# Optimization experiments

Measured on AMD Instinct MI355X. Metric: run time of the kernel, lower is better.

Reference implementation:

```python
import jax, jax.numpy as jnp
import numpy as np

GAMMA = 1.0

def setup_inputs() -> dict:
    key = jax.random.key(0)
    kq, kk, kv = jax.random.split(key, 3)
    B, N, M, D = 4, 2048, 2048, 128
    q = jax.random.normal(kq, (B, N, D), dtype=jnp.float32)
    k = jax.random.normal(kk, (B, M, D), dtype=jnp.float32)
    v = jax.random.normal(kv, (B, M, D), dtype=jnp.float32)
    return {"q": q, "k": k, "v": v}

def reference(q, k, v):
    # RBF attention: weights = softmax(-gamma * ||q_i - k_j||^2, axis=-1)
    # dist2 via expansion ||q||^2 + ||k||^2 - 2 q.k (same math as broadcast-subtract,
    # avoids materializing the [B,N,M,D] tensor the torch code builds).
    q2 = jnp.sum(q * q, axis=-1)                    # [B,N]
    k2 = jnp.sum(k * k, axis=-1)                    # [B,M]
    qk = jnp.einsum('bnd,bmd->bnm', q, k)           # [B,N,M]
    dist2 = q2[:, :, None] + k2[:, None, :] - 2.0 * qk
    weights = jax.nn.softmax(-GAMMA * dist2, axis=-1)  # [B,N,M]
    return jnp.einsum('bnm,bmd->bnd', weights, v)      # [B,N,D]
```

## Files before the change

### kernel.cpp

```cpp
#include <hip/hip_runtime.h>
#include <hip/hip_bf16.h>

#define B_ 4
#define N_ 2048
#define M_ 2048
#define D_ 128
#define QBLK 128
#define NTHREADS 256
#define KVBLK 64
#define NTILES 32
#define TILE_BYTES 16384
#define SPLIT_MAX 8
#define SCALE2LOG 2.885390081777927f
#define LOG2E 1.4426950408889634f
#define DEFER_THR 11.5424f

typedef __attribute__((ext_vector_type(8))) short short8;
typedef __attribute__((ext_vector_type(8))) _Float16 half8;
typedef __attribute__((ext_vector_type(16))) float floatx16;
typedef __attribute__((ext_vector_type(4))) unsigned int u32x4;
typedef unsigned short u16;
typedef unsigned int u32;

__device__ __forceinline__ u16 f2bf(float x) {
  u32 u = __builtin_bit_cast(u32, x);
  u32 r = (u + 0x7FFFu + ((u >> 16) & 1u)) >> 16;
  return (u16)r;
}
__device__ __forceinline__ float bf2f(u16 h) {
  u32 u = ((u32)h) << 16;
  return __builtin_bit_cast(float, u);
}
__device__ __forceinline__ u32 cvtpkh(float a, float b) {
  u32 r;
  asm("v_cvt_pkrtz_f16_f32 %0, %1, %2" : "=v"(r) : "v"(a), "v"(b));
  return r;
}

#define GLOAD16(src, dst)                                                     \
  __builtin_amdgcn_global_load_lds(                                           \
      (const __attribute__((address_space(1))) void*)(src),                   \
      (__attribute__((address_space(3))) void*)(dst), 16, 0, 0)

__global__ __launch_bounds__(256) void prep_kernel(
    const float* __restrict__ k, const float* __restrict__ v,
    u16* __restrict__ kf_g, u16* __restrict__ vt_g, float* __restrict__ k2_g)
{
  __shared__ u16 T[64][136];
  int tid = threadIdx.x;
  if (blockIdx.x < 512) {
    int gid = blockIdx.x * 256 + tid;
    int row_g = gid >> 4;
    int j = gid & 15;
    const float* kp = k + (size_t)row_g * D_ + j * 8;
    float4 a = *(const float4*)kp;
    float4 c = *(const float4*)(kp + 4);
    float xs[8] = {a.x, a.y, a.z, a.w, c.x, c.y, c.z, c.w};
    half8 kf;
    float ss = 0.f;
    #pragma unroll
    for (int e = 0; e < 8; ++e) {
      ss += xs[e] * xs[e];
      kf[e] = (_Float16)(SCALE2LOG * xs[e]);
    }
    ss += __shfl_xor(ss, 1);
    ss += __shfl_xor(ss, 2);
    ss += __shfl_xor(ss, 4);
    ss += __shfl_xor(ss, 8);
    if (j == 0) k2_g[row_g] = ss * LOG2E;
    int m = row_g & (M_ - 1);
    int b = row_g >> 11;
    int tile = m >> 6, r = m & 63;
    size_t base = ((size_t)b * NTILES + tile) * TILE_BYTES;
    u32 off = (u32)(r * 256 + j * 16) ^ ((u32)(r & 7) << 4);
    *(half8*)((char*)kf_g + base + off) = kf;
  } else {
    int blk = blockIdx.x - 512;
    int b = blk >> 5, tile = blk & 31;
    const float* vp = v + ((size_t)b * M_ + tile * 64) * D_;
    #pragma unroll
    for (int p = 0; p < 8; ++p) {
      int idx = p * 256 + tid;
      int r = idx >> 5, c4 = idx & 31;
      float4 vv = *(const float4*)(vp + (size_t)r * D_ + c4 * 4);
      T[r][c4 * 4 + 0] = __builtin_bit_cast(u16, (_Float16)vv.x);
      T[r][c4 * 4 + 1] = __builtin_bit_cast(u16, (_Float16)vv.y);
      T[r][c4 * 4 + 2] = __builtin_bit_cast(u16, (_Float16)vv.z);
      T[r][c4 * 4 + 3] = __builtin_bit_cast(u16, (_Float16)vv.w);
    }
    __syncthreads();
    size_t base = ((size_t)b * NTILES + tile) * TILE_BYTES;
    #pragma unroll
    for (int p = 0; p < 4; ++p) {
      int idx = p * 256 + tid;
      int d = idx >> 3, rb = idx & 7;
      short8 s;
      #pragma unroll
      for (int i = 0; i < 8; ++i) s[i] = (short)T[rb * 8 + i][d];
      u32 off = (u32)(d * 128 + rb * 16) ^ ((u32)(d & 7) << 4);
      *(short8*)((char*)vt_g + base + off) = s;
    }
  }
}

__global__ __launch_bounds__(NTHREADS, 2) void rbf_attn_kernel(
    const float* __restrict__ q, const u16* __restrict__ kf_g,
    const u16* __restrict__ vt_g, const float* __restrict__ k2_g,
    float* __restrict__ out, u16* __restrict__ Opart,
    float* __restrict__ mpart, float* __restrict__ lpart,
    int nsplit, int tiles_per_split)
{
  __shared__ __align__(16) u16 KfL[2][64 * 128];
  __shared__ __align__(16) u16 VtL[2][128 * 64];
  __shared__ __align__(16) float k2L[2][64];

  const int tid = threadIdx.x;
  const int w = tid >> 6;
  const int lane = tid & 63;
  const int qlc = lane & 31;
  const int h = lane >> 5;

  int b, qi, sp;
  {
    int gid = blockIdx.x;
    if (nsplit >= 2) {
      int xcd = gid & 7, slot = gid >> 3;
      int gpx = nsplit >> 1;
      int group = xcd * gpx + (slot >> 4);
      qi = slot & 15;
      b = group & 3;
      sp = group >> 2;
    } else {
      qi = gid & 15;
      b = gid >> 4;
      sp = 0;
    }
  }
  const int qt = qi;
  const int q0 = qt * QBLK;
  const int kt0 = sp * tiles_per_split, kt1 = kt0 + tiles_per_split;

  const char* kf_b = (const char*)kf_g + (size_t)b * NTILES * TILE_BYTES;
  const char* vt_b = (const char*)vt_g + (size_t)b * NTILES * TILE_BYTES;
  const float* k2_b = k2_g + (size_t)b * M_;
  const int so = tid * 16;

  #define STAGE(buf, kt)                                                      \
    do {                                                                      \
      const char* kh_ = kf_b + (size_t)(kt) * TILE_BYTES;                     \
      const char* vt_ = vt_b + (size_t)(kt) * TILE_BYTES;                     \
      char* dk = (char*)KfL[buf];                                             \
      char* dv = (char*)VtL[buf];                                             \
      _Pragma("unroll")                                                       \
      for (int c = 0; c < 4; ++c)                                             \
        GLOAD16(kh_ + c * 4096 + so, dk + c * 4096 + w * 1024);               \
      _Pragma("unroll")                                                       \
      for (int c = 0; c < 4; ++c)                                             \
        GLOAD16(vt_ + c * 4096 + so, dv + c * 4096 + w * 1024);               \
      if (tid < 16)                                                           \
        GLOAD16((const char*)(k2_b + (kt) * KVBLK) + tid * 16,                \
                (char*)k2L[buf]);                                             \
    } while (0)

  STAGE(0, kt0);

  half8 Qf[8];
  {
    const float* qp = q + ((size_t)b * N_ + q0 + w * 32 + qlc) * D_ + h * 8;
    #pragma unroll
    for (int s = 0; s < 8; ++s) {
      float4 a = *(const float4*)(qp + s * 16);
      float4 c = *(const float4*)(qp + s * 16 + 4);
      Qf[s][0] = (_Float16)a.x; Qf[s][1] = (_Float16)a.y;
      Qf[s][2] = (_Float16)a.z; Qf[s][3] = (_Float16)a.w;
      Qf[s][4] = (_Float16)c.x; Qf[s][5] = (_Float16)c.y;
      Qf[s][6] = (_Float16)c.z; Qf[s][7] = (_Float16)c.w;
    }
  }

  floatx16 o[4];
  #pragma unroll
  for (int dt = 0; dt < 4; ++dt) o[dt] = (floatx16)0.0f;
  float mrun = -1e30f, lrun = 0.f;

  asm volatile("s_waitcnt vmcnt(0)" ::: "memory");
  __syncthreads();

  int pb = 0;
  for (int kt = kt0; kt < kt1; ++kt) {
    if (kt + 1 < kt1) STAGE(pb ^ 1, kt + 1);

    const char* Kb = (const char*)KfL[pb];
    const char* Vb = (const char*)VtL[pb];
    const float* k2p = k2L[pb];

    floatx16 accS0 = (floatx16)0.0f, accS1 = (floatx16)0.0f;
    __builtin_amdgcn_s_setprio(1);
    #pragma unroll
    for (int s = 0; s < 8; ++s) {
      {
        int row = qlc;
        u32 off = ((u32)(row * 256 + s * 32 + h * 16)) ^ ((u32)(row & 7) << 4);
        half8 af = *(const half8*)(Kb + off);
        accS0 = __builtin_amdgcn_mfma_f32_32x32x16_f16(af, Qf[s], accS0, 0, 0, 0);
      }
      {
        int row = 32 + qlc;
        u32 off = ((u32)(row * 256 + s * 32 + h * 16)) ^ ((u32)(row & 7) << 4);
        half8 af = *(const half8*)(Kb + off);
        accS1 = __builtin_amdgcn_mfma_f32_32x32x16_f16(af, Qf[s], accS1, 0, 0, 0);
      }
    }
    __builtin_amdgcn_s_setprio(0);

    float mx = -3e38f;
    #pragma unroll
    for (int ct = 0; ct < 2; ++ct) {
      #pragma unroll
      for (int g = 0; g < 4; ++g) {
        float4 kq = *(const float4*)&k2p[32 * ct + 8 * g + 4 * h];
        if (ct == 0) {
          accS0[4 * g + 0] -= kq.x; accS0[4 * g + 1] -= kq.y;
          accS0[4 * g + 2] -= kq.z; accS0[4 * g + 3] -= kq.w;
          mx = fmaxf(mx, fmaxf(fmaxf(accS0[4 * g], accS0[4 * g + 1]),
                               fmaxf(accS0[4 * g + 2], accS0[4 * g + 3])));
        } else {
          accS1[4 * g + 0] -= kq.x; accS1[4 * g + 1] -= kq.y;
          accS1[4 * g + 2] -= kq.z; accS1[4 * g + 3] -= kq.w;
          mx = fmaxf(mx, fmaxf(fmaxf(accS1[4 * g], accS1[4 * g + 1]),
                               fmaxf(accS1[4 * g + 2], accS1[4 * g + 3])));
        }
      }
    }
    mx = fmaxf(mx, __shfl_xor(mx, 32));
    if (!__all(mx - mrun <= DEFER_THR)) {
      float mnew = fmaxf(mrun, mx);
      float scl = exp2f(mrun - mnew);
      mrun = mnew;
      lrun *= scl;
      #pragma unroll
      for (int i = 0; i < 16; ++i) {
        o[0][i] *= scl; o[1][i] *= scl; o[2][i] *= scl; o[3][i] *= scl;
      }
    }
    float ls = 0.f;
    u32 W[2][4][2];
    #pragma unroll
    for (int ct = 0; ct < 2; ++ct) {
      #pragma unroll
      for (int g = 0; g < 4; ++g) {
        float p0, p1, p2, p3;
        if (ct == 0) {
          p0 = exp2f(accS0[4 * g + 0] - mrun); p1 = exp2f(accS0[4 * g + 1] - mrun);
          p2 = exp2f(accS0[4 * g + 2] - mrun); p3 = exp2f(accS0[4 * g + 3] - mrun);
        } else {
          p0 = exp2f(accS1[4 * g + 0] - mrun); p1 = exp2f(accS1[4 * g + 1] - mrun);
          p2 = exp2f(accS1[4 * g + 2] - mrun); p3 = exp2f(accS1[4 * g + 3] - mrun);
        }
        ls += (p0 + p1) + (p2 + p3);
        W[ct][g][0] = cvtpkh(p0, p1);
        W[ct][g][1] = cvtpkh(p2, p3);
      }
    }
    ls += __shfl_xor(ls, 32);
    lrun += ls;

    u32 X[2][4][2];
    #pragma unroll
    for (int ct = 0; ct < 2; ++ct)
      #pragma unroll
      for (int g = 0; g < 4; ++g) {
        X[ct][g][0] = __shfl_xor(W[ct][g][0], 32);
        X[ct][g][1] = __shfl_xor(W[ct][g][1], 32);
      }

    const bool h0 = (h == 0);
    __builtin_amdgcn_s_setprio(1);
    #pragma unroll
    for (int s2 = 0; s2 < 4; ++s2) {
      const int ct = s2 >> 1, e = s2 & 1;
      u32 w0 = h0 ? W[ct][2 * e][0] : X[ct][2 * e + 1][0];
      u32 w1 = h0 ? W[ct][2 * e][1] : X[ct][2 * e + 1][1];
      u32 w2 = h0 ? X[ct][2 * e][0] : W[ct][2 * e + 1][0];
      u32 w3 = h0 ? X[ct][2 * e][1] : W[ct][2 * e + 1][1];
      half8 pf = __builtin_bit_cast(half8, (u32x4){w0, w1, w2, w3});
      #pragma unroll
      for (int dt = 0; dt < 4; ++dt) {
        int row = dt * 32 + qlc;
        u32 off = ((u32)(row * 128 + s2 * 32 + h * 16)) ^ ((u32)(row & 7) << 4);
        half8 af = *(const half8*)(Vb + off);
        o[dt] = __builtin_amdgcn_mfma_f32_32x32x16_f16(af, pf, o[dt], 0, 0, 0);
      }
    }
    __builtin_amdgcn_s_setprio(0);

    asm volatile("s_waitcnt vmcnt(0)" ::: "memory");
    __syncthreads();
    pb ^= 1;
  }

  const int qt32 = qt * 4 + w;
  if (nsplit == 1) {
    float inv = 1.0f / lrun;
    float* ob = out + ((size_t)b * N_ + q0 + w * 32 + qlc) * D_;
    #pragma unroll
    for (int dt = 0; dt < 4; ++dt)
      #pragma unroll
      for (int r = 0; r < 16; ++r) {
        int d = dt * 32 + (r & 3) + 8 * (r >> 2) + 4 * h;
        ob[d] = o[dt][r] * inv;
      }
  } else {
    u16* ob = Opart + ((((size_t)sp * B_ + b) * (N_ / 32) + qt32) * D_) * 32;
    #pragma unroll
    for (int dt = 0; dt < 4; ++dt)
      #pragma unroll
      for (int r = 0; r < 16; ++r) {
        int d = dt * 32 + (r & 3) + 8 * (r >> 2) + 4 * h;
        ob[(size_t)d * 32 + qlc] = f2bf(o[dt][r]);
      }
    if (h == 0) {
      size_t mrow = ((size_t)sp * B_ + b) * N_ + qt32 * 32 + qlc;
      mpart[mrow] = mrun;
      lpart[mrow] = lrun;
    }
  }
}

__global__ __launch_bounds__(256) void rbf_reduce_kernel(
    const u16* __restrict__ Opart, const float* __restrict__ mpart,
    const float* __restrict__ lpart, float* __restrict__ out, int nsplit)
{
  __shared__ float T[32][136];
  const int t = threadIdx.x;
  const int qln = t & 31, dg = t >> 5;
  const int b = blockIdx.x >> 6, qt32 = blockIdx.x & 63;
  const size_t stride = (size_t)B_ * N_;
  const size_t mbase = (size_t)b * N_ + qt32 * 32 + qln;
  float mmax = -3e38f;
  for (int s = 0; s < nsplit; ++s)
    mmax = fmaxf(mmax, mpart[s * stride + mbase]);
  float acc[16];
  #pragma unroll
  for (int i = 0; i < 16; ++i) acc[i] = 0.f;
  float lsum = 0.f;
  for (int s = 0; s < nsplit; ++s) {
    float wv = exp2f(mpart[s * stride + mbase] - mmax);
    lsum += wv * lpart[s * stride + mbase];
    const u16* ob = Opart +
        ((((size_t)s * B_ + b) * (N_ / 32) + qt32) * D_ + dg * 16) * 32 + qln;
    #pragma unroll
    for (int dd = 0; dd < 16; ++dd) acc[dd] += wv * bf2f(ob[(size_t)dd * 32]);
  }
  float inv = 1.0f / lsum;
  #pragma unroll
  for (int dd = 0; dd < 16; ++dd) T[qln][dg * 16 + dd] = acc[dd] * inv;
  __syncthreads();
  const int r = t >> 3, seg = t & 7;
  float* op = out + ((size_t)b * N_ + qt32 * 32 + r) * D_ + seg * 16;
  #pragma unroll
  for (int i = 0; i < 4; ++i) {
    float4 v4 = {T[r][seg * 16 + 4 * i], T[r][seg * 16 + 4 * i + 1],
                 T[r][seg * 16 + 4 * i + 2], T[r][seg * 16 + 4 * i + 3]};
    *(float4*)(op + 4 * i) = v4;
  }
}

extern "C" void kernel_launch(void* const* d_in, const int* in_sizes, int n_in,
                              void* d_out, int out_size, void* d_ws, size_t ws_size,
                              hipStream_t stream) {
  const float* q = (const float*)d_in[0];
  const float* k = (const float*)d_in[1];
  const float* v = (const float*)d_in[2];
  float* out = (float*)d_out;

  const size_t tileBytesAll = (size_t)B_ * NTILES * TILE_BYTES;
  u16* kf_g = (u16*)d_ws;
  u16* vt_g = (u16*)((char*)d_ws + tileBytesAll);
  float* k2_g = (float*)((char*)d_ws + 2 * tileBytesAll);
  const size_t prepBytes = 2 * tileBytesAll + (size_t)B_ * M_ * sizeof(float);

  const size_t perO = (size_t)B_ * N_ * D_ * sizeof(u16);
  const size_t perML = 2 * (size_t)B_ * N_ * sizeof(float);
  int nsplit = SPLIT_MAX;
  while (nsplit > 1 && prepBytes + (size_t)nsplit * (perO + perML) > ws_size)
    nsplit >>= 1;

  u16* Opart = (u16*)((char*)d_ws + prepBytes);
  float* mpart = (float*)((char*)d_ws + prepBytes + (size_t)nsplit * perO);
  float* lpart = mpart + (size_t)nsplit * B_ * N_;
  int tiles_per_split = NTILES / nsplit;

  prep_kernel<<<512 + B_ * NTILES, 256, 0, stream>>>(k, v, kf_g, vt_g, k2_g);

  rbf_attn_kernel<<<dim3(16 * B_ * nsplit), NTHREADS, 0, stream>>>(
      q, kf_g, vt_g, k2_g, out, Opart, mpart, lpart, nsplit, tiles_per_split);
  if (nsplit > 1) {
    rbf_reduce_kernel<<<B_ * (N_ / 32), 256, 0, stream>>>(
        Opart, mpart, lpart, out, nsplit);
  }
}
```

Baseline: 39.47 us.

## Load K and V fragments directly from global into registers, dropping LDS staging

The prep kernel now writes K and V^T tiles in a lane-contiguous fragment layout, so each lane of the attention kernel can read its MFMA operands straight from global memory (L2) into registers. LDS double buffering, the block-wide barriers and the LDS reads are removed. K for the next tile is prefetched after the PV MFMAs and V is loaded after the QK MFMAs into the same register array. This trades LDS traffic and synchronization for redundant global/L2 reads across the four waves and exposed load latency, since only one register buffer is reused.

Measured after the change: 40.63 us. 2.9% more time.

```diff
diff --git a/kernel.cpp b/kernel.cpp
--- a/kernel.cpp
+++ b/kernel.cpp
@@ -36,11 +36,6 @@
   asm("v_cvt_pkrtz_f16_f32 %0, %1, %2" : "=v"(r) : "v"(a), "v"(b));
   return r;
 }
-
-#define GLOAD16(src, dst)                                                     \
-  __builtin_amdgcn_global_load_lds(                                           \
-      (const __attribute__((address_space(1))) void*)(src),                   \
-      (__attribute__((address_space(3))) void*)(dst), 16, 0, 0)
 
 __global__ __launch_bounds__(256) void prep_kernel(
     const float* __restrict__ k, const float* __restrict__ v,
@@ -72,7 +67,8 @@
     int b = row_g >> 11;
     int tile = m >> 6, r = m & 63;
     size_t base = ((size_t)b * NTILES + tile) * TILE_BYTES;
-    u32 off = (u32)(r * 256 + j * 16) ^ ((u32)(r & 7) << 4);
+    u32 off = (u32)((r >> 5) * 8192 + (j >> 1) * 1024 +
+                    (((r & 31) + 32 * (j & 1)) * 16));
     *(half8*)((char*)kf_g + base + off) = kf;
   } else {
     int blk = blockIdx.x - 512;
@@ -89,7 +85,7 @@
       T[r][c4 * 4 + 3] = __builtin_bit_cast(u16, (_Float16)vv.w);
     }
     __syncthreads();
-    size_t base = ((size_t)b * NTILES + tile) * TILE_BYTES;
+    size_t base = (size_t)blk * TILE_BYTES;
     #pragma unroll
     for (int p = 0; p < 4; ++p) {
       int idx = p * 256 + tid;
@@ -97,7 +93,8 @@
       short8 s;
       #pragma unroll
       for (int i = 0; i < 8; ++i) s[i] = (short)T[rb * 8 + i][d];
-      u32 off = (u32)(d * 128 + rb * 16) ^ ((u32)(d & 7) << 4);
+      u32 off = (u32)((d >> 5) * 4096 + (rb >> 1) * 1024 +
+                      (((d & 31) + 32 * (rb & 1)) * 16));
       *(short8*)((char*)vt_g + base + off) = s;
     }
   }
@@ -110,10 +107,6 @@
     float* __restrict__ mpart, float* __restrict__ lpart,
     int nsplit, int tiles_per_split)
 {
-  __shared__ __align__(16) u16 KfL[2][64 * 128];
-  __shared__ __align__(16) u16 VtL[2][128 * 64];
-  __shared__ __align__(16) float k2L[2][64];
-
   const int tid = threadIdx.x;
   const int w = tid >> 6;
   const int lane = tid & 63;
@@ -143,26 +136,33 @@
   const char* kf_b = (const char*)kf_g + (size_t)b * NTILES * TILE_BYTES;
   const char* vt_b = (const char*)vt_g + (size_t)b * NTILES * TILE_BYTES;
   const float* k2_b = k2_g + (size_t)b * M_;
-  const int so = tid * 16;
-
-  #define STAGE(buf, kt)                                                      \
+
+  u32x4 kv[16];
+  float4 k2v[2][4];
+
+  #define LOADK(kt)                                                           \
     do {                                                                      \
-      const char* kh_ = kf_b + (size_t)(kt) * TILE_BYTES;                     \
-      const char* vt_ = vt_b + (size_t)(kt) * TILE_BYTES;                     \
-      char* dk = (char*)KfL[buf];                                             \
-      char* dv = (char*)VtL[buf];                                             \
+      const char* kb_ = kf_b + (size_t)(kt) * TILE_BYTES;                     \
       _Pragma("unroll")                                                       \
-      for (int c = 0; c < 4; ++c)                                             \
-        GLOAD16(kh_ + c * 4096 + so, dk + c * 4096 + w * 1024);               \
+      for (int i = 0; i < 16; ++i)                                            \
+        kv[i] = *(const u32x4*)(kb_ + i * 1024 + lane * 16);                  \
+      const float* kp_ = k2_b + (kt) * KVBLK + 4 * h;                         \
       _Pragma("unroll")                                                       \
-      for (int c = 0; c < 4; ++c)                                             \
-        GLOAD16(vt_ + c * 4096 + so, dv + c * 4096 + w * 1024);               \
-      if (tid < 16)                                                           \
-        GLOAD16((const char*)(k2_b + (kt) * KVBLK) + tid * 16,                \
-                (char*)k2L[buf]);                                             \
+      for (int ct = 0; ct < 2; ++ct)                                          \
+        _Pragma("unroll")                                                     \
+        for (int g = 0; g < 4; ++g)                                           \
+          k2v[ct][g] = *(const float4*)(kp_ + 32 * ct + 8 * g);               \
     } while (0)
 
-  STAGE(0, kt0);
+  #define LOADV(kt)                                                           \
+    do {                                                                      \
+      const char* vb_ = vt_b + (size_t)(kt) * TILE_BYTES;                     \
+      _Pragma("unroll")                                                       \
+      for (int i = 0; i < 16; ++i)                                            \
+        kv[i] = *(const u32x4*)(vb_ + i * 1024 + lane * 16);                  \
+    } while (0)
+
+  LOADK(kt0);
 
   half8 Qf[8];
   {
@@ -183,54 +183,36 @@
   for (int dt = 0; dt < 4; ++dt) o[dt] = (floatx16)0.0f;
   float mrun = -1e30f, lrun = 0.f;
 
-  asm volatile("s_waitcnt vmcnt(0)" ::: "memory");
-  __syncthreads();
-
-  int pb = 0;
   for (int kt = kt0; kt < kt1; ++kt) {
-    if (kt + 1 < kt1) STAGE(pb ^ 1, kt + 1);
-
-    const char* Kb = (const char*)KfL[pb];
-    const char* Vb = (const char*)VtL[pb];
-    const float* k2p = k2L[pb];
-
     floatx16 accS0 = (floatx16)0.0f, accS1 = (floatx16)0.0f;
     __builtin_amdgcn_s_setprio(1);
     #pragma unroll
     for (int s = 0; s < 8; ++s) {
-      {
-        int row = qlc;
-        u32 off = ((u32)(row * 256 + s * 32 + h * 16)) ^ ((u32)(row & 7) << 4);
-        half8 af = *(const half8*)(Kb + off);
-        accS0 = __builtin_amdgcn_mfma_f32_32x32x16_f16(af, Qf[s], accS0, 0, 0, 0);
-      }
-      {
-        int row = 32 + qlc;
-        u32 off = ((u32)(row * 256 + s * 32 + h * 16)) ^ ((u32)(row & 7) << 4);
-        half8 af = *(const half8*)(Kb + off);
-        accS1 = __builtin_amdgcn_mfma_f32_32x32x16_f16(af, Qf[s], accS1, 0, 0, 0);
-      }
+      half8 a0 = __builtin_bit_cast(half8, kv[s]);
+      half8 a1 = __builtin_bit_cast(half8, kv[8 + s]);
+      accS0 = __builtin_amdgcn_mfma_f32_32x32x16_f16(a0, Qf[s], accS0, 0, 0, 0);
+      accS1 = __builtin_amdgcn_mfma_f32_32x32x16_f16(a1, Qf[s], accS1, 0, 0, 0);
     }
     __builtin_amdgcn_s_setprio(0);
 
+    LOADV(kt);
+
     float mx = -3e38f;
     #pragma unroll
-    for (int ct = 0; ct < 2; ++ct) {
-      #pragma unroll
-      for (int g = 0; g < 4; ++g) {
-        float4 kq = *(const float4*)&k2p[32 * ct + 8 * g + 4 * h];
-        if (ct == 0) {
-          accS0[4 * g + 0] -= kq.x; accS0[4 * g + 1] -= kq.y;
-          accS0[4 * g + 2] -= kq.z; accS0[4 * g + 3] -= kq.w;
-          mx = fmaxf(mx, fmaxf(fmaxf(accS0[4 * g], accS0[4 * g + 1]),
-                               fmaxf(accS0[4 * g + 2], accS0[4 * g + 3])));
-        } else {
-          accS1[4 * g + 0] -= kq.x; accS1[4 * g + 1] -= kq.y;
-          accS1[4 * g + 2] -= kq.z; accS1[4 * g + 3] -= kq.w;
-          mx = fmaxf(mx, fmaxf(fmaxf(accS1[4 * g], accS1[4 * g + 1]),
-                               fmaxf(accS1[4 * g + 2], accS1[4 * g + 3])));
-        }
-      }
+    for (int g = 0; g < 4; ++g) {
+      float4 kq = k2v[0][g];
+      accS0[4 * g + 0] -= kq.x; accS0[4 * g + 1] -= kq.y;
+      accS0[4 * g + 2] -= kq.z; accS0[4 * g + 3] -= kq.w;
+      mx = fmaxf(mx, fmaxf(fmaxf(accS0[4 * g], accS0[4 * g + 1]),
+                           fmaxf(accS0[4 * g + 2], accS0[4 * g + 3])));
+    }
+    #pragma unroll
+    for (int g = 0; g < 4; ++g) {
+      float4 kq = k2v[1][g];
+      accS1[4 * g + 0] -= kq.x; accS1[4 * g + 1] -= kq.y;
+      accS1[4 * g + 2] -= kq.z; accS1[4 * g + 3] -= kq.w;
+      mx = fmaxf(mx, fmaxf(fmaxf(accS1[4 * g], accS1[4 * g + 1]),
+                           fmaxf(accS1[4 * g + 2], accS1[4 * g + 3])));
     }
     mx = fmaxf(mx, __shfl_xor(mx, 32));
     if (!__all(mx - mrun <= DEFER_THR)) {
@@ -246,21 +228,24 @@
     float ls = 0.f;
     u32 W[2][4][2];
     #pragma unroll
-    for (int ct = 0; ct < 2; ++ct) {
-      #pragma unroll
-      for (int g = 0; g < 4; ++g) {
-        float p0, p1, p2, p3;
-        if (ct == 0) {
-          p0 = exp2f(accS0[4 * g + 0] - mrun); p1 = exp2f(accS0[4 * g + 1] - mrun);
-          p2 = exp2f(accS0[4 * g + 2] - mrun); p3 = exp2f(accS0[4 * g + 3] - mrun);
-        } else {
-          p0 = exp2f(accS1[4 * g + 0] - mrun); p1 = exp2f(accS1[4 * g + 1] - mrun);
-          p2 = exp2f(accS1[4 * g + 2] - mrun); p3 = exp2f(accS1[4 * g + 3] - mrun);
-        }
-        ls += (p0 + p1) + (p2 + p3);
-        W[ct][g][0] = cvtpkh(p0, p1);
-        W[ct][g][1] = cvtpkh(p2, p3);
-      }
+    for (int g = 0; g < 4; ++g) {
+      float p0 = exp2f(accS0[4 * g + 0] - mrun);
+      float p1 = exp2f(accS0[4 * g + 1] - mrun);
+      float p2 = exp2f(accS0[4 * g + 2] - mrun);
+      float p3 = exp2f(accS0[4 * g + 3] - mrun);
+      ls += (p0 + p1) + (p2 + p3);
+      W[0][g][0] = cvtpkh(p0, p1);
+      W[0][g][1] = cvtpkh(p2, p3);
+    }
+    #pragma unroll
+    for (int g = 0; g < 4; ++g) {
+      float p0 = exp2f(accS1[4 * g + 0] - mrun);
+      float p1 = exp2f(accS1[4 * g + 1] - mrun);
+      float p2 = exp2f(accS1[4 * g + 2] - mrun);
+      float p3 = exp2f(accS1[4 * g + 3] - mrun);
+      ls += (p0 + p1) + (p2 + p3);
+      W[1][g][0] = cvtpkh(p0, p1);
+      W[1][g][1] = cvtpkh(p2, p3);
     }
     ls += __shfl_xor(ls, 32);
     lrun += ls;
@@ -286,17 +271,13 @@
       half8 pf = __builtin_bit_cast(half8, (u32x4){w0, w1, w2, w3});
       #pragma unroll
       for (int dt = 0; dt < 4; ++dt) {
-        int row = dt * 32 + qlc;
-        u32 off = ((u32)(row * 128 + s2 * 32 + h * 16)) ^ ((u32)(row & 7) << 4);
-        half8 af = *(const half8*)(Vb + off);
+        half8 af = __builtin_bit_cast(half8, kv[dt * 4 + s2]);
         o[dt] = __builtin_amdgcn_mfma_f32_32x32x16_f16(af, pf, o[dt], 0, 0, 0);
       }
     }
     __builtin_amdgcn_s_setprio(0);
 
-    asm volatile("s_waitcnt vmcnt(0)" ::: "memory");
-    __syncthreads();
-    pb ^= 1;
+    if (kt + 1 < kt1) LOADK(kt + 1);
   }
 
   const int qt32 = qt * 4 + w;
@@ -325,6 +306,8 @@
       lpart[mrow] = lrun;
     }
   }
+  #undef LOADK
+  #undef LOADV
 }
 
 __global__ __launch_bounds__(256) void rbf_reduce_kernel(
```

## Fuse split-KV reduction into attention kernel via last-block atomic counter

Applied to the files above, without the earlier changes.

Removes the separate reduce kernel launch. Each attention block bumps a per-(batch, query-tile) atomic counter after writing its partial output and softmax stats. The block that arrives last merges all splits for its four 32-row groups, using its now-free LDS as staging. The counter is zeroed in the prep kernel. This saves a kernel launch and the gap between kernels, but puts the merge work on a few tail blocks and adds fences and atomics.

Measured after the change: 126.0 us. +219.1%, slower.

```diff
diff --git a/kernel.cpp b/kernel.cpp
--- a/kernel.cpp
+++ b/kernel.cpp
@@ -44,10 +44,12 @@
 
 __global__ __launch_bounds__(256) void prep_kernel(
     const float* __restrict__ k, const float* __restrict__ v,
-    u16* __restrict__ kf_g, u16* __restrict__ vt_g, float* __restrict__ k2_g)
+    u16* __restrict__ kf_g, u16* __restrict__ vt_g, float* __restrict__ k2_g,
+    int* __restrict__ cnt_g)
 {
   __shared__ u16 T[64][136];
   int tid = threadIdx.x;
+  if (blockIdx.x == 0 && tid < 64) cnt_g[tid] = 0;
   if (blockIdx.x < 512) {
     int gid = blockIdx.x * 256 + tid;
     int row_g = gid >> 4;
@@ -89,7 +91,7 @@
       T[r][c4 * 4 + 3] = __builtin_bit_cast(u16, (_Float16)vv.w);
     }
     __syncthreads();
-    size_t base = ((size_t)b * NTILES + tile) * TILE_BYTES;
+    size_t base = (size_t)blk * TILE_BYTES;
     #pragma unroll
     for (int p = 0; p < 4; ++p) {
       int idx = p * 256 + tid;
@@ -100,6 +102,44 @@
       u32 off = (u32)(d * 128 + rb * 16) ^ ((u32)(d & 7) << 4);
       *(short8*)((char*)vt_g + base + off) = s;
     }
+  }
+}
+
+__device__ __forceinline__ void merge_group(
+    int b, int qt32, float* __restrict__ T, const u16* __restrict__ Opart,
+    const float* __restrict__ mpart, const float* __restrict__ lpart,
+    float* __restrict__ out, int nsplit)
+{
+  const int t = threadIdx.x;
+  const int qln = t & 31, dg = t >> 5;
+  const size_t stride = (size_t)B_ * N_;
+  const size_t mbase = (size_t)b * N_ + qt32 * 32 + qln;
+  float mmax = -3e38f;
+  for (int s = 0; s < nsplit; ++s)
+    mmax = fmaxf(mmax, mpart[s * stride + mbase]);
+  float acc[16];
+  #pragma unroll
+  for (int i = 0; i < 16; ++i) acc[i] = 0.f;
+  float lsum = 0.f;
+  for (int s = 0; s < nsplit; ++s) {
+    float wv = exp2f(mpart[s * stride + mbase] - mmax);
+    lsum += wv * lpart[s * stride + mbase];
+    const u16* ob = Opart +
+        ((((size_t)s * B_ + b) * (N_ / 32) + qt32) * D_ + dg * 16) * 32 + qln;
+    #pragma unroll
+    for (int dd = 0; dd < 16; ++dd) acc[dd] += wv * bf2f(ob[(size_t)dd * 32]);
+  }
+  float inv = 1.0f / lsum;
+  #pragma unroll
+  for (int dd = 0; dd < 16; ++dd) T[qln * 136 + dg * 16 + dd] = acc[dd] * inv;
+  __syncthreads();
+  const int r = t >> 3, seg = t & 7;
+  float* op = out + ((size_t)b * N_ + qt32 * 32 + r) * D_ + seg * 16;
+  #pragma unroll
+  for (int i = 0; i < 4; ++i) {
+    float4 v4 = {T[r * 136 + seg * 16 + 4 * i], T[r * 136 + seg * 16 + 4 * i + 1],
+                 T[r * 136 + seg * 16 + 4 * i + 2], T[r * 136 + seg * 16 + 4 * i + 3]};
+    *(float4*)(op + 4 * i) = v4;
   }
 }
 
@@ -108,11 +148,12 @@
     const u16* __restrict__ vt_g, const float* __restrict__ k2_g,
     float* __restrict__ out, u16* __restrict__ Opart,
     float* __restrict__ mpart, float* __restrict__ lpart,
-    int nsplit, int tiles_per_split)
+    int* __restrict__ cnt_g, int nsplit, int tiles_per_split)
 {
-  __shared__ __align__(16) u16 KfL[2][64 * 128];
-  __shared__ __align__(16) u16 VtL[2][128 * 64];
+  __shared__ __align__(16) u16 KfL[2][8192];
+  __shared__ __align__(16) u16 VtL[2][8192];
   __shared__ __align__(16) float k2L[2][64];
+  __shared__ int lastflag;
 
   const int tid = threadIdx.x;
   const int w = tid >> 6;
@@ -310,7 +351,10 @@
         int d = dt * 32 + (r & 3) + 8 * (r >> 2) + 4 * h;
         ob[d] = o[dt][r] * inv;
       }
-  } else {
+    return;
+  }
+
+  {
     u16* ob = Opart + ((((size_t)sp * B_ + b) * (N_ / 32) + qt32) * D_) * 32;
     #pragma unroll
     for (int dt = 0; dt < 4; ++dt)
@@ -325,45 +369,24 @@
       lpart[mrow] = lrun;
     }
   }
-}
-
-__global__ __launch_bounds__(256) void rbf_reduce_kernel(
-    const u16* __restrict__ Opart, const float* __restrict__ mpart,
-    const float* __restrict__ lpart, float* __restrict__ out, int nsplit)
-{
-  __shared__ float T[32][136];
-  const int t = threadIdx.x;
-  const int qln = t & 31, dg = t >> 5;
-  const int b = blockIdx.x >> 6, qt32 = blockIdx.x & 63;
-  const size_t stride = (size_t)B_ * N_;
-  const size_t mbase = (size_t)b * N_ + qt32 * 32 + qln;
-  float mmax = -3e38f;
-  for (int s = 0; s < nsplit; ++s)
-    mmax = fmaxf(mmax, mpart[s * stride + mbase]);
-  float acc[16];
-  #pragma unroll
-  for (int i = 0; i < 16; ++i) acc[i] = 0.f;
-  float lsum = 0.f;
-  for (int s = 0; s < nsplit; ++s) {
-    float wv = exp2f(mpart[s * stride + mbase] - mmax);
-    lsum += wv * lpart[s * stride + mbase];
-    const u16* ob = Opart +
-        ((((size_t)s * B_ + b) * (N_ / 32) + qt32) * D_ + dg * 16) * 32 + qln;
-    #pragma unroll
-    for (int dd = 0; dd < 16; ++dd) acc[dd] += wv * bf2f(ob[(size_t)dd * 32]);
-  }
-  float inv = 1.0f / lsum;
-  #pragma unroll
-  for (int dd = 0; dd < 16; ++dd) T[qln][dg * 16 + dd] = acc[dd] * inv;
+
+  __threadfence();
   __syncthreads();
-  const int r = t >> 3, seg = t & 7;
-  float* op = out + ((size_t)b * N_ + qt32 * 32 + r) * D_ + seg * 16;
-  #pragma unroll
-  for (int i = 0; i < 4; ++i) {
-    float4 v4 = {T[r][seg * 16 + 4 * i], T[r][seg * 16 + 4 * i + 1],
-                 T[r][seg * 16 + 4 * i + 2], T[r][seg * 16 + 4 * i + 3]};
-    *(float4*)(op + 4 * i) = v4;
-  }
+  if (tid == 0) {
+    int old = atomicAdd(cnt_g + (b * 16 + qt), 1);
+    lastflag = (old == nsplit - 1);
+  }
+  __syncthreads();
+  if (lastflag) {
+    __threadfence();
+    float* T = (float*)KfL;
+    #pragma unroll
+    for (int j = 0; j < 4; ++j) {
+      __syncthreads();
+      merge_group(b, qt * 4 + j, T, Opart, mpart, lpart, out, nsplit);
+    }
+  }
+  #undef STAGE
 }
 
 extern "C" void kernel_launch(void* const* d_in, const int* in_sizes, int n_in,
@@ -382,21 +405,22 @@
 
   const size_t perO = (size_t)B_ * N_ * D_ * sizeof(u16);
   const size_t perML = 2 * (size_t)B_ * N_ * sizeof(float);
+  const size_t cntBytes = 256;
   int nsplit = SPLIT_MAX;
-  while (nsplit > 1 && prepBytes + (size_t)nsplit * (perO + perML) > ws_size)
+  while (nsplit > 1 &&
+         prepBytes + (size_t)nsplit * (perO + perML) + cntBytes > ws_size)
     nsplit >>= 1;
 
   u16* Opart = (u16*)((char*)d_ws + prepBytes);
   float* mpart = (float*)((char*)d_ws + prepBytes + (size_t)nsplit * perO);
   float* lpart = mpart + (size_t)nsplit * B_ * N_;
+  int* cnt_g = (int*)(lpart + (size_t)nsplit * B_ * N_);
   int tiles_per_split = NTILES / nsplit;
 
-  prep_kernel<<<512 + B_ * NTILES, 256, 0, stream>>>(k, v, kf_g, vt_g, k2_g);
+  prep_kernel<<<512 + B_ * NTILES, 256, 0, stream>>>(k, v, kf_g, vt_g, k2_g,
+                                                     cnt_g);
 
   rbf_attn_kernel<<<dim3(16 * B_ * nsplit), NTHREADS, 0, stream>>>(
-      q, kf_g, vt_g, k2_g, out, Opart, mpart, lpart, nsplit, tiles_per_split);
-  if (nsplit > 1) {
-    rbf_reduce_kernel<<<B_ * (N_ / 32), 256, 0, stream>>>(
-        Opart, mpart, lpart, out, nsplit);
-  }
-}
+      q, kf_g, vt_g, k2_g, out, Opart, mpart, lpart, cnt_g, nsplit,
+      tiles_per_split);
+}
```

## Halve K tile height, decouple V staging, and raise split count and occupancy

Applied to the files above, without the earlier changes.

K tiles shrink to 32 rows so each iteration does one score MFMA chain instead of two. V tiles stay at 64 rows and are double-buffered separately, staged every other iteration with a column offset picking the half to use. Split-K maximum doubles to 16 and launch bounds ask for 3 blocks per CU, to get more blocks in flight and better latency hiding from a smaller LDS footprint. The cost is more partial outputs for the reduce kernel to write and read, and a larger workspace; if the workspace is too small the split count falls back.

Result: slower. 48.04 us (+21.7%).

```diff
diff --git a/kernel.cpp b/kernel.cpp
--- a/kernel.cpp
+++ b/kernel.cpp
@@ -7,10 +7,11 @@
 #define D_ 128
 #define QBLK 128
 #define NTHREADS 256
-#define KVBLK 64
-#define NTILES 32
-#define TILE_BYTES 16384
-#define SPLIT_MAX 8
+#define NKTILES 64
+#define KT_BYTES 8192
+#define NVTILES 32
+#define VT_BYTES 16384
+#define SPLIT_MAX 16
 #define SCALE2LOG 2.885390081777927f
 #define LOG2E 1.4426950408889634f
 #define DEFER_THR 11.5424f
@@ -70,8 +71,8 @@
     if (j == 0) k2_g[row_g] = ss * LOG2E;
     int m = row_g & (M_ - 1);
     int b = row_g >> 11;
-    int tile = m >> 6, r = m & 63;
-    size_t base = ((size_t)b * NTILES + tile) * TILE_BYTES;
+    int tile = m >> 5, r = m & 31;
+    size_t base = ((size_t)b * NKTILES + tile) * KT_BYTES;
     u32 off = (u32)(r * 256 + j * 16) ^ ((u32)(r & 7) << 4);
     *(half8*)((char*)kf_g + base + off) = kf;
   } else {
@@ -89,7 +90,7 @@
       T[r][c4 * 4 + 3] = __builtin_bit_cast(u16, (_Float16)vv.w);
     }
     __syncthreads();
-    size_t base = ((size_t)b * NTILES + tile) * TILE_BYTES;
+    size_t base = (size_t)blk * VT_BYTES;
     #pragma unroll
     for (int p = 0; p < 4; ++p) {
       int idx = p * 256 + tid;
@@ -103,16 +104,16 @@
   }
 }
 
-__global__ __launch_bounds__(NTHREADS, 2) void rbf_attn_kernel(
+__global__ __launch_bounds__(NTHREADS, 3) void rbf_attn_kernel(
     const float* __restrict__ q, const u16* __restrict__ kf_g,
     const u16* __restrict__ vt_g, const float* __restrict__ k2_g,
     float* __restrict__ out, u16* __restrict__ Opart,
     float* __restrict__ mpart, float* __restrict__ lpart,
     int nsplit, int tiles_per_split)
 {
-  __shared__ __align__(16) u16 KfL[2][64 * 128];
+  __shared__ __align__(16) u16 KfL[2][32 * 128];
   __shared__ __align__(16) u16 VtL[2][128 * 64];
-  __shared__ __align__(16) float k2L[2][64];
+  __shared__ __align__(16) float k2L[2][32];
 
   const int tid = threadIdx.x;
   const int w = tid >> 6;
@@ -138,31 +139,36 @@
   }
   const int qt = qi;
   const int q0 = qt * QBLK;
-  const int kt0 = sp * tiles_per_split, kt1 = kt0 + tiles_per_split;
-
-  const char* kf_b = (const char*)kf_g + (size_t)b * NTILES * TILE_BYTES;
-  const char* vt_b = (const char*)vt_g + (size_t)b * NTILES * TILE_BYTES;
+  const int kt0 = sp * tiles_per_split;
+  const int tps = tiles_per_split;
+
+  const char* kf_b = (const char*)kf_g + (size_t)b * NKTILES * KT_BYTES;
+  const char* vt_b = (const char*)vt_g + (size_t)b * NVTILES * VT_BYTES;
   const float* k2_b = k2_g + (size_t)b * M_;
   const int so = tid * 16;
 
-  #define STAGE(buf, kt)                                                      \
+  #define STAGE_K(buf, kt)                                                    \
     do {                                                                      \
-      const char* kh_ = kf_b + (size_t)(kt) * TILE_BYTES;                     \
-      const char* vt_ = vt_b + (size_t)(kt) * TILE_BYTES;                     \
+      const char* kh_ = kf_b + (size_t)(kt) * KT_BYTES;                       \
       char* dk = (char*)KfL[buf];                                             \
+      GLOAD16(kh_ + so, dk + w * 1024);                                       \
+      GLOAD16(kh_ + 4096 + so, dk + 4096 + w * 1024);                         \
+      if (tid < 8)                                                            \
+        GLOAD16((const char*)(k2_b + (kt) * 32) + tid * 16,                   \
+                (char*)k2L[buf]);                                             \
+    } while (0)
+
+  #define STAGE_V(buf, vt)                                                    \
+    do {                                                                      \
+      const char* vt_ = vt_b + (size_t)(vt) * VT_BYTES;                       \
       char* dv = (char*)VtL[buf];                                             \
       _Pragma("unroll")                                                       \
       for (int c = 0; c < 4; ++c)                                             \
-        GLOAD16(kh_ + c * 4096 + so, dk + c * 4096 + w * 1024);               \
-      _Pragma("unroll")                                                       \
-      for (int c = 0; c < 4; ++c)                                             \
         GLOAD16(vt_ + c * 4096 + so, dv + c * 4096 + w * 1024);               \
-      if (tid < 16)                                                           \
-        GLOAD16((const char*)(k2_b + (kt) * KVBLK) + tid * 16,                \
-                (char*)k2L[buf]);                                             \
     } while (0)
 
-  STAGE(0, kt0);
+  STAGE_K(0, kt0);
+  STAGE_V(0, kt0 >> 1);
 
   half8 Qf[8];
   {
@@ -186,51 +192,33 @@
   asm volatile("s_waitcnt vmcnt(0)" ::: "memory");
   __syncthreads();
 
-  int pb = 0;
-  for (int kt = kt0; kt < kt1; ++kt) {
-    if (kt + 1 < kt1) STAGE(pb ^ 1, kt + 1);
+  int pb = 0, vb = 0;
+  for (int i = 0; i < tps; ++i) {
+    const int kt = kt0 + i;
+    if (((i & 1) == 0) && (i + 2 < tps)) STAGE_V(vb ^ 1, (kt >> 1) + 1);
+    if (i + 1 < tps) STAGE_K(pb ^ 1, kt + 1);
 
     const char* Kb = (const char*)KfL[pb];
-    const char* Vb = (const char*)VtL[pb];
     const float* k2p = k2L[pb];
 
-    floatx16 accS0 = (floatx16)0.0f, accS1 = (floatx16)0.0f;
+    floatx16 accS = (floatx16)0.0f;
     __builtin_amdgcn_s_setprio(1);
     #pragma unroll
     for (int s = 0; s < 8; ++s) {
-      {
-        int row = qlc;
-        u32 off = ((u32)(row * 256 + s * 32 + h * 16)) ^ ((u32)(row & 7) << 4);
-        half8 af = *(const half8*)(Kb + off);
-        accS0 = __builtin_amdgcn_mfma_f32_32x32x16_f16(af, Qf[s], accS0, 0, 0, 0);
-      }
-      {
-        int row = 32 + qlc;
-        u32 off = ((u32)(row * 256 + s * 32 + h * 16)) ^ ((u32)(row & 7) << 4);
-        half8 af = *(const half8*)(Kb + off);
-        accS1 = __builtin_amdgcn_mfma_f32_32x32x16_f16(af, Qf[s], accS1, 0, 0, 0);
-      }
+      u32 off = ((u32)(qlc * 256 + s * 32 + h * 16)) ^ ((u32)(qlc & 7) << 4);
+      half8 af = *(const half8*)(Kb + off);
+      accS = __builtin_amdgcn_mfma_f32_32x32x16_f16(af, Qf[s], accS, 0, 0, 0);
     }
     __builtin_amdgcn_s_setprio(0);
 
     float mx = -3e38f;
     #pragma unroll
-    for (int ct = 0; ct < 2; ++ct) {
-      #pragma unroll
-      for (int g = 0; g < 4; ++g) {
-        float4 kq = *(const float4*)&k2p[32 * ct + 8 * g + 4 * h];
-        if (ct == 0) {
-          accS0[4 * g + 0] -= kq.x; accS0[4 * g + 1] -= kq.y;
-          accS0[4 * g + 2] -= kq.z; accS0[4 * g + 3] -= kq.w;
-          mx = fmaxf(mx, fmaxf(fmaxf(accS0[4 * g], accS0[4 * g + 1]),
-                               fmaxf(accS0[4 * g + 2], accS0[4 * g + 3])));
-        } else {
-          accS1[4 * g + 0] -= kq.x; accS1[4 * g + 1] -= kq.y;
-          accS1[4 * g + 2] -= kq.z; accS1[4 * g + 3] -= kq.w;
-          mx = fmaxf(mx, fmaxf(fmaxf(accS1[4 * g], accS1[4 * g + 1]),
-                               fmaxf(accS1[4 * g + 2], accS1[4 * g + 3])));
-        }
-      }
+    for (int g = 0; g < 4; ++g) {
+      float4 kq = *(const float4*)&k2p[8 * g + 4 * h];
+      accS[4 * g + 0] -= kq.x; accS[4 * g + 1] -= kq.y;
+      accS[4 * g + 2] -= kq.z; accS[4 * g + 3] -= kq.w;
+      mx = fmaxf(mx, fmaxf(fmaxf(accS[4 * g], accS[4 * g + 1]),
+                           fmaxf(accS[4 * g + 2], accS[4 * g + 3])));
     }
     mx = fmaxf(mx, __shfl_xor(mx, 32));
     if (!__all(mx - mrun <= DEFER_THR)) {
@@ -239,55 +227,48 @@
       mrun = mnew;
       lrun *= scl;
       #pragma unroll
-      for (int i = 0; i < 16; ++i) {
-        o[0][i] *= scl; o[1][i] *= scl; o[2][i] *= scl; o[3][i] *= scl;
+      for (int j = 0; j < 16; ++j) {
+        o[0][j] *= scl; o[1][j] *= scl; o[2][j] *= scl; o[3][j] *= scl;
       }
     }
     float ls = 0.f;
-    u32 W[2][4][2];
-    #pragma unroll
-    for (int ct = 0; ct < 2; ++ct) {
-      #pragma unroll
-      for (int g = 0; g < 4; ++g) {
-        float p0, p1, p2, p3;
-        if (ct == 0) {
-          p0 = exp2f(accS0[4 * g + 0] - mrun); p1 = exp2f(accS0[4 * g + 1] - mrun);
-          p2 = exp2f(accS0[4 * g + 2] - mrun); p3 = exp2f(accS0[4 * g + 3] - mrun);
-        } else {
-          p0 = exp2f(accS1[4 * g + 0] - mrun); p1 = exp2f(accS1[4 * g + 1] - mrun);
-          p2 = exp2f(accS1[4 * g + 2] - mrun); p3 = exp2f(accS1[4 * g + 3] - mrun);
-        }
-        ls += (p0 + p1) + (p2 + p3);
-        W[ct][g][0] = cvtpkh(p0, p1);
-        W[ct][g][1] = cvtpkh(p2, p3);
-      }
+    u32 W[4][2];
+    #pragma unroll
+    for (int g = 0; g < 4; ++g) {
+      float p0 = exp2f(accS[4 * g + 0] - mrun);
+      float p1 = exp2f(accS[4 * g + 1] - mrun);
+      float p2 = exp2f(accS[4 * g + 2] - mrun);
+      float p3 = exp2f(accS[4 * g + 3] - mrun);
+      ls += (p0 + p1) + (p2 + p3);
+      W[g][0] = cvtpkh(p0, p1);
+      W[g][1] = cvtpkh(p2, p3);
     }
     ls += __shfl_xor(ls, 32);
     lrun += ls;
 
-    u32 X[2][4][2];
-    #pragma unroll
-    for (int ct = 0; ct < 2; ++ct)
-      #pragma unroll
-      for (int g = 0; g < 4; ++g) {
-        X[ct][g][0] = __shfl_xor(W[ct][g][0], 32);
-        X[ct][g][1] = __shfl_xor(W[ct][g][1], 32);
-      }
+    u32 X[4][2];
+    #pragma unroll
+    for (int g = 0; g < 4; ++g) {
+      X[g][0] = __shfl_xor(W[g][0], 32);
+      X[g][1] = __shfl_xor(W[g][1], 32);
+    }
 
     const bool h0 = (h == 0);
+    const char* Vb = (const char*)VtL[vb];
+    const u32 colb = (u32)(kt & 1) * 64;
     __builtin_amdgcn_s_setprio(1);
     #pragma unroll
-    for (int s2 = 0; s2 < 4; ++s2) {
-      const int ct = s2 >> 1, e = s2 & 1;
-      u32 w0 = h0 ? W[ct][2 * e][0] : X[ct][2 * e + 1][0];
-      u32 w1 = h0 ? W[ct][2 * e][1] : X[ct][2 * e + 1][1];
-      u32 w2 = h0 ? X[ct][2 * e][0] : W[ct][2 * e + 1][0];
-      u32 w3 = h0 ? X[ct][2 * e][1] : W[ct][2 * e + 1][1];
+    for (int s2 = 0; s2 < 2; ++s2) {
+      u32 w0 = h0 ? W[2 * s2][0] : X[2 * s2 + 1][0];
+      u32 w1 = h0 ? W[2 * s2][1] : X[2 * s2 + 1][1];
+      u32 w2 = h0 ? X[2 * s2][0] : W[2 * s2 + 1][0];
+      u32 w3 = h0 ? X[2 * s2][1] : W[2 * s2 + 1][1];
       half8 pf = __builtin_bit_cast(half8, (u32x4){w0, w1, w2, w3});
       #pragma unroll
       for (int dt = 0; dt < 4; ++dt) {
         int row = dt * 32 + qlc;
-        u32 off = ((u32)(row * 128 + s2 * 32 + h * 16)) ^ ((u32)(row & 7) << 4);
+        u32 off = ((u32)(row * 128) + colb + s2 * 32 + h * 16) ^
+                  ((u32)(row & 7) << 4);
         half8 af = *(const half8*)(Vb + off);
         o[dt] = __builtin_amdgcn_mfma_f32_32x32x16_f16(af, pf, o[dt], 0, 0, 0);
       }
@@ -297,6 +278,7 @@
     asm volatile("s_waitcnt vmcnt(0)" ::: "memory");
     __syncthreads();
     pb ^= 1;
+    if (i & 1) vb ^= 1;
   }
 
   const int qt32 = qt * 4 + w;
@@ -325,6 +307,8 @@
       lpart[mrow] = lrun;
     }
   }
+  #undef STAGE_K
+  #undef STAGE_V
 }
 
 __global__ __launch_bounds__(256) void rbf_reduce_kernel(
@@ -374,11 +358,12 @@
   const float* v = (const float*)d_in[2];
   float* out = (float*)d_out;
 
-  const size_t tileBytesAll = (size_t)B_ * NTILES * TILE_BYTES;
+  const size_t kfBytes = (size_t)B_ * NKTILES * KT_BYTES;
+  const size_t vtBytes = (size_t)B_ * NVTILES * VT_BYTES;
   u16* kf_g = (u16*)d_ws;
-  u16* vt_g = (u16*)((char*)d_ws + tileBytesAll);
-  float* k2_g = (float*)((char*)d_ws + 2 * tileBytesAll);
-  const size_t prepBytes = 2 * tileBytesAll + (size_t)B_ * M_ * sizeof(float);
+  u16* vt_g = (u16*)((char*)d_ws + kfBytes);
+  float* k2_g = (float*)((char*)d_ws + kfBytes + vtBytes);
+  const size_t prepBytes = kfBytes + vtBytes + (size_t)B_ * M_ * sizeof(float);
 
   const size_t perO = (size_t)B_ * N_ * D_ * sizeof(u16);
   const size_t perML = 2 * (size_t)B_ * N_ * sizeof(float);
@@ -389,9 +374,9 @@
   u16* Opart = (u16*)((char*)d_ws + prepBytes);
   float* mpart = (float*)((char*)d_ws + prepBytes + (size_t)nsplit * perO);
   float* lpart = mpart + (size_t)nsplit * B_ * N_;
-  int tiles_per_split = NTILES / nsplit;
-
-  prep_kernel<<<512 + B_ * NTILES, 256, 0, stream>>>(k, v, kf_g, vt_g, k2_g);
+  int tiles_per_split = NKTILES / nsplit;
+
+  prep_kernel<<<512 + B_ * NVTILES, 256, 0, stream>>>(k, v, kf_g, vt_g, k2_g);
 
   rbf_attn_kernel<<<dim3(16 * B_ * nsplit), NTHREADS, 0, stream>>>(
       q, kf_g, vt_g, k2_g, out, Opart, mpart, lpart, nsplit, tiles_per_split);
```
